# Optimization experiments

Hardware: AMD Instinct MI355X
Metric: run time of the kernel (lower is better)

## Reference

```python
import jax, jax.numpy as jnp
import numpy as np

XD = 64      # input_size
D = 512      # encoding_size
R = 512      # hidden_size (WFA rank)
MIX = 8      # mixture components
WIN = 4096   # window_size
INIT_STD = 0.1


def setup_inputs() -> dict:
    key = jax.random.key(0)
    ks = jax.random.split(key, 16)
    s = INIT_STD

    def lin(k, fan_out, fan_in):
        lim = 1.0 / np.sqrt(fan_in)
        kw, kb = jax.random.split(k)
        W = jax.random.uniform(kw, (fan_out, fan_in), jnp.float32, -lim, lim)
        b = jax.random.uniform(kb, (fan_out,), jnp.float32, -lim, lim)
        return W, b

    W1, b1 = lin(ks[3], D, XD)            # encoder_1: xd -> d
    W2, b2 = lin(ks[4], D, D)             # encoder_2: d -> d
    Wmu, bmu = lin(ks[5], MIX * XD, R)    # mu_out
    Wmu2, bmu2 = lin(ks[6], MIX * XD, MIX * XD)  # mu_out2
    Wsig, bsig = lin(ks[7], MIX * XD, R)  # sig_out
    Wal, bal = lin(ks[8], MIX, R)         # alpha_out

    return {
        "X": jax.random.normal(ks[0], (WIN, XD), jnp.float32),
        "prev": jax.nn.softmax(jax.random.uniform(ks[1], (1, R), jnp.float32), axis=1),
        "A": s * jax.random.normal(ks[2], (R, D, R), jnp.float32),
        "W1": W1, "b1": b1, "W2": W2, "b2": b2,
        "Wmu": Wmu, "bmu": bmu, "Wmu2": Wmu2, "bmu2": bmu2,
        "Wsig": Wsig, "bsig": bsig, "Wal": Wal, "bal": bal,
    }


def reference(X, prev, A, W1, b1, W2, b2, Wmu, bmu, Wmu2, bmu2, Wsig, bsig, Wal, bal):
    # prev is never updated inside the torch window loop, so all window_size-1
    # steps share the same prev -> vectorize over the window dimension T.
    cur = X[:-1]            # [T, xd]
    nxt = X[1:]             # [T, xd]

    # encoder: two linears with relu
    e = jax.nn.relu(cur @ W1.T + b1)        # [T, d]
    e = jax.nn.relu(e @ W2.T + b2)          # [T, d]

    # WFA transition: einsum('d,i,idj->j', enc_t, prev, A) for every t.
    # Contract prev with A once into a [d, r] transition matrix.
    B = jnp.einsum('i,idj->dj', prev.ravel(), A)   # [d, r]
    h = jax.nn.sigmoid(e @ B)                       # [T, r]

    # phi: mixture-density head evaluating log p(next | h)
    mu = ((h @ Wmu.T + bmu) @ Wmu2.T + bmu2).reshape(-1, MIX, XD)  # [T, K, xd]
    sig = jnp.exp(h @ Wsig.T + bsig).reshape(-1, MIX, XD)          # [T, K, xd]
    log_alpha = jax.nn.log_softmax(h @ Wal.T + bal, axis=-1)       # [T, K]

    z = (nxt[:, None, :] - mu) / sig
    log_comp = (-0.5 * jnp.sum(z * z, axis=-1)
                - jnp.sum(jnp.log(sig), axis=-1)
                - 0.5 * XD * jnp.log(2.0 * jnp.pi))                # [T, K]
    ll = jax.nn.logsumexp(log_alpha + log_comp, axis=-1)           # [T]

    # torch forward returns only the last step's result and the last hidden
    # state (detached) as the new prev.
    return ll[-1:], jax.lax.stop_gradient(h[-1:])
```

## Files before the change

### kernel.cpp

```cpp
#include <hip/hip_runtime.h>
#include <math.h>

#define NSLOT    8
#define WS_E     0
#define WS_E1    512
#define WS_HPRE  1024
#define WS_H     (WS_HPRE + NSLOT*512)
#define WS_T1    (WS_H + 512)
#define WS_SP    (WS_T1 + 512)
#define WS_MU    (WS_SP + 512)
#define WS_AL    (WS_MU + 512)

__global__ __launch_bounds__(256) void k_e1(const float* __restrict__ X,
    const float* __restrict__ W1, const float* __restrict__ b1,
    float* __restrict__ ws)
{
    int t = threadIdx.x, b = blockIdx.x;
    int w = t >> 6, l = t & 63;
    int r = b * 4 + w;
    float s = W1[(size_t)r * 64 + l] * X[4094 * 64 + l];
#pragma unroll
    for (int off = 32; off > 0; off >>= 1) s += __shfl_down(s, off);
    if (l == 0) ws[WS_E1 + r] = fmaxf(s + b1[r], 0.f);
    int gid = b * 256 + t;
    if (gid < NSLOT * 512) ws[WS_HPRE + gid] = 0.f;
}

__global__ __launch_bounds__(64) void k_e2(const float* __restrict__ W2,
    const float* __restrict__ b2, float* __restrict__ ws)
{
    int r = blockIdx.x, l = threadIdx.x;
    const float4* w4 = (const float4*)(W2 + (size_t)r * 512);
    const float4* x4 = (const float4*)(ws + WS_E1);
    float4 w0 = w4[2*l], w1 = w4[2*l+1];
    float4 x0 = x4[2*l], x1 = x4[2*l+1];
    float s = w0.x*x0.x + w0.y*x0.y + w0.z*x0.z + w0.w*x0.w
            + w1.x*x1.x + w1.y*x1.y + w1.z*x1.z + w1.w*x1.w;
#pragma unroll
    for (int off = 32; off > 0; off >>= 1) s += __shfl_down(s, off);
    if (l == 0) ws[WS_E + r] = fmaxf(s + b2[r], 0.f);
}

__global__ __launch_bounds__(256) void k_contract(const float* __restrict__ A,
    const float* __restrict__ prev, float* __restrict__ ws)
{
    __shared__ float cvals[136];
    __shared__ unsigned short idxs[136];
    __shared__ int cnts[2];
    __shared__ float4 comb[128];

    int t = threadIdx.x;
    int b = blockIdx.x;
    int i = b >> 2;
    int d0 = (b & 3) << 7;
    const float* e = ws + WS_E;

    float c = 0.f; bool nz = false;
    if (t < 128) {
        c = prev[i] * e[d0 + t];
        nz = (c != 0.f);
    }
    unsigned long long bm = __ballot(nz);
    int lane = t & 63;
    int w = t >> 6;
    if (t < 128 && lane == 0) cnts[w] = __popcll(bm);
    __syncthreads();
    if (nz) {
        int pos = __popcll(bm & ((1ull << lane) - 1)) + (w ? cnts[0] : 0);
        idxs[pos] = (unsigned short)t;
        cvals[pos] = c;
    }
    int nnz = cnts[0] + cnts[1];
    int nnzp = (nnz + 7) & ~7;
    if (t < 8 && nnz + t < nnzp) {
        cvals[nnz + t] = 0.f;
        idxs[nnz + t] = 0;
    }
    __syncthreads();

    int g  = t >> 7;
    int jj = t & 127;
    const float* Abase = A + ((size_t)i * 512 + d0) * 512 + (size_t)jj * 4;
    float4 acc = make_float4(0.f, 0.f, 0.f, 0.f);

#pragma unroll 2
    for (int k = g; k + 6 < nnzp; k += 8) {
        int dA = idxs[k], dB = idxs[k+2], dC = idxs[k+4], dD = idxs[k+6];
        float cA = cvals[k], cB = cvals[k+2], cC = cvals[k+4], cD = cvals[k+6];
        float4 a0 = *(const float4*)(Abase + ((size_t)dA << 9));
        float4 a1 = *(const float4*)(Abase + ((size_t)dB << 9));
        float4 a2 = *(const float4*)(Abase + ((size_t)dC << 9));
        float4 a3 = *(const float4*)(Abase + ((size_t)dD << 9));
        acc.x = fmaf(cA, a0.x, acc.x); acc.y = fmaf(cA, a0.y, acc.y);
        acc.z = fmaf(cA, a0.z, acc.z); acc.w = fmaf(cA, a0.w, acc.w);
        acc.x = fmaf(cB, a1.x, acc.x); acc.y = fmaf(cB, a1.y, acc.y);
        acc.z = fmaf(cB, a1.z, acc.z); acc.w = fmaf(cB, a1.w, acc.w);
        acc.x = fmaf(cC, a2.x, acc.x); acc.y = fmaf(cC, a2.y, acc.y);
        acc.z = fmaf(cC, a2.z, acc.z); acc.w = fmaf(cC, a2.w, acc.w);
        acc.x = fmaf(cD, a3.x, acc.x); acc.y = fmaf(cD, a3.y, acc.y);
        acc.z = fmaf(cD, a3.z, acc.z); acc.w = fmaf(cD, a3.w, acc.w);
    }

    if (g == 1) comb[jj] = acc;
    __syncthreads();
    if (g == 0) {
        float4 o = comb[jj];
        float* hp = ws + WS_HPRE + (size_t)(b & (NSLOT - 1)) * 512;
        int j = jj * 4;
        atomicAdd(&hp[j],     acc.x + o.x);
        atomicAdd(&hp[j + 1], acc.y + o.y);
        atomicAdd(&hp[j + 2], acc.z + o.z);
        atomicAdd(&hp[j + 3], acc.w + o.w);
    }
}

__global__ __launch_bounds__(512) void k_h(float* __restrict__ ws, float* __restrict__ out)
{
    int t = threadIdx.x;
    float s = 0.f;
#pragma unroll
    for (int s2 = 0; s2 < NSLOT; ++s2) s += ws[WS_HPRE + s2 * 512 + t];
    float h = 1.f / (1.f + expf(-s));
    ws[WS_H + t] = h;
    out[1 + t] = h;
}

__global__ __launch_bounds__(64) void k_mv3(const float* __restrict__ Wmu, const float* __restrict__ bmu,
    const float* __restrict__ Wsig, const float* __restrict__ bsig,
    const float* __restrict__ Wal, const float* __restrict__ bal,
    float* __restrict__ ws)
{
    int r = blockIdx.x;
    const float* Wrow; float bias; float* outp;
    if (r < 512)       { Wrow = Wmu  + (size_t)r * 512;          bias = bmu[r];          outp = ws + WS_T1 + r; }
    else if (r < 1024) { int rr = r - 512;  Wrow = Wsig + (size_t)rr * 512; bias = bsig[rr]; outp = ws + WS_SP + rr; }
    else               { int rr = r - 1024; Wrow = Wal  + (size_t)rr * 512; bias = bal[rr];  outp = ws + WS_AL + rr; }
    int l = threadIdx.x;
    const float4* W4 = (const float4*)Wrow;
    const float4* h4 = (const float4*)(ws + WS_H);
    float4 w0 = W4[2*l], w1 = W4[2*l+1];
    float4 h0 = h4[2*l], h1 = h4[2*l+1];
    float s = w0.x*h0.x + w0.y*h0.y + w0.z*h0.z + w0.w*h0.w
            + w1.x*h1.x + w1.y*h1.y + w1.z*h1.z + w1.w*h1.w;
#pragma unroll
    for (int off = 32; off > 0; off >>= 1) s += __shfl_down(s, off);
    if (l == 0) *outp = s + bias;
}

__global__ __launch_bounds__(64) void k_mv1(const float* __restrict__ W, const float* __restrict__ bvec,
    float* __restrict__ ws)
{
    int r = blockIdx.x;
    int l = threadIdx.x;
    const float4* W4 = (const float4*)(W + (size_t)r * 512);
    const float4* x4 = (const float4*)(ws + WS_T1);
    float4 w0 = W4[2*l], w1 = W4[2*l+1];
    float4 x0 = x4[2*l], x1 = x4[2*l+1];
    float s = w0.x*x0.x + w0.y*x0.y + w0.z*x0.z + w0.w*x0.w
            + w1.x*x1.x + w1.y*x1.y + w1.z*x1.z + w1.w*x1.w;
#pragma unroll
    for (int off = 32; off > 0; off >>= 1) s += __shfl_down(s, off);
    if (l == 0) ws[WS_MU + r] = s + bvec[r];
}

__global__ __launch_bounds__(512) void k_final(const float* __restrict__ X,
    float* __restrict__ ws, float* __restrict__ out)
{
    __shared__ float lc[8];
    int t = threadIdx.x;
    int m = t >> 6, x = t & 63;
    float nx = X[4095 * 64 + x];
    float mu = ws[WS_MU + t];
    float sp = ws[WS_SP + t];
    float z  = (nx - mu) * expf(-sp);
    float v  = 0.5f * z * z + sp;
#pragma unroll
    for (int off = 32; off > 0; off >>= 1) v += __shfl_down(v, off);
    if (x == 0) lc[m] = -v - 58.812066125099056f;
    __syncthreads();
    if (t == 0) {
        float al[8], g[8];
        float mx1 = -1e30f, mx2 = -1e30f;
#pragma unroll
        for (int q = 0; q < 8; ++q) {
            al[q] = ws[WS_AL + q];
            g[q]  = al[q] + lc[q];
            mx1 = fmaxf(mx1, al[q]);
            mx2 = fmaxf(mx2, g[q]);
        }
        float s1 = 0.f, s2 = 0.f;
#pragma unroll
        for (int q = 0; q < 8; ++q) { s1 += expf(al[q] - mx1); s2 += expf(g[q] - mx2); }
        out[0] = (mx2 + logf(s2)) - (mx1 + logf(s1));
    }
}

extern "C" void kernel_launch(void* const* d_in, const int* in_sizes, int n_in,
                              void* d_out, int out_size, void* d_ws, size_t ws_size,
                              hipStream_t stream)
{
    const float* X    = (const float*)d_in[0];
    const float* prev = (const float*)d_in[1];
    const float* A    = (const float*)d_in[2];
    const float* W1   = (const float*)d_in[3];
    const float* b1   = (const float*)d_in[4];
    const float* W2   = (const float*)d_in[5];
    const float* b2   = (const float*)d_in[6];
    const float* Wmu  = (const float*)d_in[7];
    const float* bmu  = (const float*)d_in[8];
    const float* Wmu2 = (const float*)d_in[9];
    const float* bmu2 = (const float*)d_in[10];
    const float* Wsig = (const float*)d_in[11];
    const float* bsig = (const float*)d_in[12];
    const float* Wal  = (const float*)d_in[13];
    const float* bal  = (const float*)d_in[14];
    float* out = (float*)d_out;
    float* ws  = (float*)d_ws;

    hipLaunchKernelGGL(k_e1,       dim3(128),  dim3(256), 0, stream, X, W1, b1, ws);
    hipLaunchKernelGGL(k_e2,       dim3(512),  dim3(64),  0, stream, W2, b2, ws);
    hipLaunchKernelGGL(k_contract, dim3(2048), dim3(256), 0, stream, A, prev, ws);
    hipLaunchKernelGGL(k_h,        dim3(1),    dim3(512), 0, stream, ws, out);
    hipLaunchKernelGGL(k_mv3,      dim3(1032), dim3(64),  0, stream, Wmu, bmu, Wsig, bsig, Wal, bal, ws);
    hipLaunchKernelGGL(k_mv1,      dim3(512),  dim3(64),  0, stream, Wmu2, bmu2, ws);
    hipLaunchKernelGGL(k_final,    dim3(1),    dim3(512), 0, stream, X, ws, out);
}
```

Before: 75.98 us.

## Fuse sigmoid into head matvec and final reduction into mu2 via atomics

```diff
diff --git a/kernel.cpp b/kernel.cpp
--- a/kernel.cpp
+++ b/kernel.cpp
@@ -1,15 +1,18 @@
 #include <hip/hip_runtime.h>
 #include <math.h>
+
+typedef float f32x4 __attribute__((ext_vector_type(4)));
 
 #define NSLOT    8
 #define WS_E     0
 #define WS_E1    512
 #define WS_HPRE  1024
-#define WS_H     (WS_HPRE + NSLOT*512)
-#define WS_T1    (WS_H + 512)
+#define WS_LC    (WS_HPRE + NSLOT*512)
+#define WS_CNT   (WS_LC + 8)
+#define WS_T1    (WS_CNT + 8)
 #define WS_SP    (WS_T1 + 512)
-#define WS_MU    (WS_SP + 512)
-#define WS_AL    (WS_MU + 512)
+#define WS_AL    (WS_SP + 512)
+#define WS_ZLEN  (NSLOT*512 + 16)
 
 __global__ __launch_bounds__(256) void k_e1(const float* __restrict__ X,
     const float* __restrict__ W1, const float* __restrict__ b1,
@@ -23,13 +26,15 @@
     for (int off = 32; off > 0; off >>= 1) s += __shfl_down(s, off);
     if (l == 0) ws[WS_E1 + r] = fmaxf(s + b1[r], 0.f);
     int gid = b * 256 + t;
-    if (gid < NSLOT * 512) ws[WS_HPRE + gid] = 0.f;
-}
-
-__global__ __launch_bounds__(64) void k_e2(const float* __restrict__ W2,
+    if (gid < WS_ZLEN) ws[WS_HPRE + gid] = 0.f;
+}
+
+__global__ __launch_bounds__(256) void k_e2(const float* __restrict__ W2,
     const float* __restrict__ b2, float* __restrict__ ws)
 {
-    int r = blockIdx.x, l = threadIdx.x;
+    int t = threadIdx.x, b = blockIdx.x;
+    int w = t >> 6, l = t & 63;
+    int r = b * 4 + w;
     const float4* w4 = (const float4*)(W2 + (size_t)r * 512);
     const float4* x4 = (const float4*)(ws + WS_E1);
     float4 w0 = w4[2*l], w1 = w4[2*l+1];
@@ -44,10 +49,10 @@
 __global__ __launch_bounds__(256) void k_contract(const float* __restrict__ A,
     const float* __restrict__ prev, float* __restrict__ ws)
 {
-    __shared__ float cvals[136];
-    __shared__ unsigned short idxs[136];
+    __shared__ float cvals[160];
+    __shared__ unsigned short idxs[160];
     __shared__ int cnts[2];
-    __shared__ float4 comb[128];
+    __shared__ float comb[512];
 
     int t = threadIdx.x;
     int b = blockIdx.x;
@@ -71,8 +76,8 @@
         cvals[pos] = c;
     }
     int nnz = cnts[0] + cnts[1];
-    int nnzp = (nnz + 7) & ~7;
-    if (t < 8 && nnz + t < nnzp) {
+    int nnzp = (nnz + 15) & ~15;
+    if (t < 16 && nnz + t < nnzp) {
         cvals[nnz + t] = 0.f;
         idxs[nnz + t] = 0;
     }
@@ -81,77 +86,81 @@
     int g  = t >> 7;
     int jj = t & 127;
     const float* Abase = A + ((size_t)i * 512 + d0) * 512 + (size_t)jj * 4;
-    float4 acc = make_float4(0.f, 0.f, 0.f, 0.f);
-
-#pragma unroll 2
-    for (int k = g; k + 6 < nnzp; k += 8) {
-        int dA = idxs[k], dB = idxs[k+2], dC = idxs[k+4], dD = idxs[k+6];
-        float cA = cvals[k], cB = cvals[k+2], cC = cvals[k+4], cD = cvals[k+6];
-        float4 a0 = *(const float4*)(Abase + ((size_t)dA << 9));
-        float4 a1 = *(const float4*)(Abase + ((size_t)dB << 9));
-        float4 a2 = *(const float4*)(Abase + ((size_t)dC << 9));
-        float4 a3 = *(const float4*)(Abase + ((size_t)dD << 9));
-        acc.x = fmaf(cA, a0.x, acc.x); acc.y = fmaf(cA, a0.y, acc.y);
-        acc.z = fmaf(cA, a0.z, acc.z); acc.w = fmaf(cA, a0.w, acc.w);
-        acc.x = fmaf(cB, a1.x, acc.x); acc.y = fmaf(cB, a1.y, acc.y);
-        acc.z = fmaf(cB, a1.z, acc.z); acc.w = fmaf(cB, a1.w, acc.w);
-        acc.x = fmaf(cC, a2.x, acc.x); acc.y = fmaf(cC, a2.y, acc.y);
-        acc.z = fmaf(cC, a2.z, acc.z); acc.w = fmaf(cC, a2.w, acc.w);
-        acc.x = fmaf(cD, a3.x, acc.x); acc.y = fmaf(cD, a3.y, acc.y);
-        acc.z = fmaf(cD, a3.z, acc.z); acc.w = fmaf(cD, a3.w, acc.w);
-    }
-
-    if (g == 1) comb[jj] = acc;
+    f32x4 acc = (f32x4)0.f;
+
+    for (int k = g; k + 14 < nnzp; k += 16) {
+        int i0 = idxs[k],    i1 = idxs[k+2],  i2 = idxs[k+4],  i3 = idxs[k+6];
+        int i4 = idxs[k+8],  i5 = idxs[k+10], i6 = idxs[k+12], i7 = idxs[k+14];
+        float c0 = cvals[k],    c1 = cvals[k+2],  c2 = cvals[k+4],  c3 = cvals[k+6];
+        float c4 = cvals[k+8],  c5 = cvals[k+10], c6 = cvals[k+12], c7 = cvals[k+14];
+        f32x4 a0 = __builtin_nontemporal_load((const f32x4*)(Abase + ((size_t)i0 << 9)));
+        f32x4 a1 = __builtin_nontemporal_load((const f32x4*)(Abase + ((size_t)i1 << 9)));
+        f32x4 a2 = __builtin_nontemporal_load((const f32x4*)(Abase + ((size_t)i2 << 9)));
+        f32x4 a3 = __builtin_nontemporal_load((const f32x4*)(Abase + ((size_t)i3 << 9)));
+        f32x4 a4 = __builtin_nontemporal_load((const f32x4*)(Abase + ((size_t)i4 << 9)));
+        f32x4 a5 = __builtin_nontemporal_load((const f32x4*)(Abase + ((size_t)i5 << 9)));
+        f32x4 a6 = __builtin_nontemporal_load((const f32x4*)(Abase + ((size_t)i6 << 9)));
+        f32x4 a7 = __builtin_nontemporal_load((const f32x4*)(Abase + ((size_t)i7 << 9)));
+        acc += c0 * a0; acc += c1 * a1; acc += c2 * a2; acc += c3 * a3;
+        acc += c4 * a4; acc += c5 * a5; acc += c6 * a6; acc += c7 * a7;
+    }
+
+    if (g == 1) { ((f32x4*)comb)[jj] = acc; }
     __syncthreads();
     if (g == 0) {
-        float4 o = comb[jj];
+        f32x4 o = ((f32x4*)comb)[jj];
+        acc += o;
         float* hp = ws + WS_HPRE + (size_t)(b & (NSLOT - 1)) * 512;
         int j = jj * 4;
-        atomicAdd(&hp[j],     acc.x + o.x);
-        atomicAdd(&hp[j + 1], acc.y + o.y);
-        atomicAdd(&hp[j + 2], acc.z + o.z);
-        atomicAdd(&hp[j + 3], acc.w + o.w);
-    }
-}
-
-__global__ __launch_bounds__(512) void k_h(float* __restrict__ ws, float* __restrict__ out)
-{
-    int t = threadIdx.x;
-    float s = 0.f;
-#pragma unroll
-    for (int s2 = 0; s2 < NSLOT; ++s2) s += ws[WS_HPRE + s2 * 512 + t];
-    float h = 1.f / (1.f + expf(-s));
-    ws[WS_H + t] = h;
-    out[1 + t] = h;
-}
-
-__global__ __launch_bounds__(64) void k_mv3(const float* __restrict__ Wmu, const float* __restrict__ bmu,
+        atomicAdd(&hp[j],     acc.x);
+        atomicAdd(&hp[j + 1], acc.y);
+        atomicAdd(&hp[j + 2], acc.z);
+        atomicAdd(&hp[j + 3], acc.w);
+    }
+}
+
+__global__ __launch_bounds__(64) void k_post1(const float* __restrict__ Wmu, const float* __restrict__ bmu,
     const float* __restrict__ Wsig, const float* __restrict__ bsig,
     const float* __restrict__ Wal, const float* __restrict__ bal,
-    float* __restrict__ ws)
-{
+    float* __restrict__ ws, float* __restrict__ out)
+{
+    __shared__ float h[512];
+    int t = threadIdx.x;
+#pragma unroll
+    for (int q = 0; q < 8; ++q) {
+        int j = q * 64 + t;
+        float s = 0.f;
+#pragma unroll
+        for (int s2 = 0; s2 < NSLOT; ++s2) s += ws[WS_HPRE + s2 * 512 + j];
+        h[j] = 1.f / (1.f + expf(-s));
+    }
+    __syncthreads();
+
     int r = blockIdx.x;
+    if (r == 1032) {
+#pragma unroll
+        for (int q = 0; q < 8; ++q) { int j = q * 64 + t; out[1 + j] = h[j]; }
+        return;
+    }
     const float* Wrow; float bias; float* outp;
-    if (r < 512)       { Wrow = Wmu  + (size_t)r * 512;          bias = bmu[r];          outp = ws + WS_T1 + r; }
+    if (r < 512)       { Wrow = Wmu  + (size_t)r * 512;           bias = bmu[r];           outp = ws + WS_T1 + r; }
     else if (r < 1024) { int rr = r - 512;  Wrow = Wsig + (size_t)rr * 512; bias = bsig[rr]; outp = ws + WS_SP + rr; }
     else               { int rr = r - 1024; Wrow = Wal  + (size_t)rr * 512; bias = bal[rr];  outp = ws + WS_AL + rr; }
-    int l = threadIdx.x;
     const float4* W4 = (const float4*)Wrow;
-    const float4* h4 = (const float4*)(ws + WS_H);
-    float4 w0 = W4[2*l], w1 = W4[2*l+1];
-    float4 h0 = h4[2*l], h1 = h4[2*l+1];
+    const float4* h4 = (const float4*)h;
+    float4 w0 = W4[2*t], w1 = W4[2*t+1];
+    float4 h0 = h4[2*t], h1 = h4[2*t+1];
     float s = w0.x*h0.x + w0.y*h0.y + w0.z*h0.z + w0.w*h0.w
             + w1.x*h1.x + w1.y*h1.y + w1.z*h1.z + w1.w*h1.w;
 #pragma unroll
     for (int off = 32; off > 0; off >>= 1) s += __shfl_down(s, off);
-    if (l == 0) *outp = s + bias;
-}
-
-__global__ __launch_bounds__(64) void k_mv1(const float* __restrict__ W, const float* __restrict__ bvec,
-    float* __restrict__ ws)
-{
-    int r = blockIdx.x;
-    int l = threadIdx.x;
+    if (t == 0) *outp = s + bias;
+}
+
+__global__ __launch_bounds__(64) void k_mu_final(const float* __restrict__ W, const float* __restrict__ bvec,
+    const float* __restrict__ X, float* __restrict__ ws, float* __restrict__ out)
+{
+    int r = blockIdx.x, l = threadIdx.x;
     const float4* W4 = (const float4*)(W + (size_t)r * 512);
     const float4* x4 = (const float4*)(ws + WS_T1);
     float4 w0 = W4[2*l], w1 = W4[2*l+1];
@@ -160,38 +169,31 @@
             + w1.x*x1.x + w1.y*x1.y + w1.z*x1.z + w1.w*x1.w;
 #pragma unroll
     for (int off = 32; off > 0; off >>= 1) s += __shfl_down(s, off);
-    if (l == 0) ws[WS_MU + r] = s + bvec[r];
-}
-
-__global__ __launch_bounds__(512) void k_final(const float* __restrict__ X,
-    float* __restrict__ ws, float* __restrict__ out)
-{
-    __shared__ float lc[8];
-    int t = threadIdx.x;
-    int m = t >> 6, x = t & 63;
-    float nx = X[4095 * 64 + x];
-    float mu = ws[WS_MU + t];
-    float sp = ws[WS_SP + t];
-    float z  = (nx - mu) * expf(-sp);
-    float v  = 0.5f * z * z + sp;
-#pragma unroll
-    for (int off = 32; off > 0; off >>= 1) v += __shfl_down(v, off);
-    if (x == 0) lc[m] = -v - 58.812066125099056f;
-    __syncthreads();
-    if (t == 0) {
-        float al[8], g[8];
-        float mx1 = -1e30f, mx2 = -1e30f;
-#pragma unroll
-        for (int q = 0; q < 8; ++q) {
-            al[q] = ws[WS_AL + q];
-            g[q]  = al[q] + lc[q];
-            mx1 = fmaxf(mx1, al[q]);
-            mx2 = fmaxf(mx2, g[q]);
+    if (l == 0) {
+        float mu = s + bvec[r];
+        int m = r >> 6, x = r & 63;
+        float nx = X[4095 * 64 + x];
+        float sp = ws[WS_SP + r];
+        float z  = (nx - mu) * expf(-sp);
+        atomicAdd(&ws[WS_LC + m], -(0.5f * z * z + sp));
+        __threadfence();
+        unsigned int done = atomicAdd((unsigned int*)(ws + WS_CNT), 1u);
+        if (done == 511) {
+            float al[8], g[8];
+            float mx1 = -1e30f, mx2 = -1e30f;
+#pragma unroll
+            for (int q = 0; q < 8; ++q) {
+                al[q] = ws[WS_AL + q];
+                float lc = atomicAdd(&ws[WS_LC + q], 0.f) - 58.812066125099056f;
+                g[q] = al[q] + lc;
+                mx1 = fmaxf(mx1, al[q]);
+                mx2 = fmaxf(mx2, g[q]);
+            }
+            float s1 = 0.f, s2 = 0.f;
+#pragma unroll
+            for (int q = 0; q < 8; ++q) { s1 += expf(al[q] - mx1); s2 += expf(g[q] - mx2); }
+            out[0] = (mx2 + logf(s2)) - (mx1 + logf(s1));
         }
-        float s1 = 0.f, s2 = 0.f;
-#pragma unroll
-        for (int q = 0; q < 8; ++q) { s1 += expf(al[q] - mx1); s2 += expf(g[q] - mx2); }
-        out[0] = (mx2 + logf(s2)) - (mx1 + logf(s1));
     }
 }
 
@@ -218,10 +220,8 @@
     float* ws  = (float*)d_ws;
 
     hipLaunchKernelGGL(k_e1,       dim3(128),  dim3(256), 0, stream, X, W1, b1, ws);
-    hipLaunchKernelGGL(k_e2,       dim3(512),  dim3(64),  0, stream, W2, b2, ws);
+    hipLaunchKernelGGL(k_e2,       dim3(128),  dim3(256), 0, stream, W2, b2, ws);
     hipLaunchKernelGGL(k_contract, dim3(2048), dim3(256), 0, stream, A, prev, ws);
-    hipLaunchKernelGGL(k_h,        dim3(1),    dim3(512), 0, stream, ws, out);
-    hipLaunchKernelGGL(k_mv3,      dim3(1032), dim3(64),  0, stream, Wmu, bmu, Wsig, bsig, Wal, bal, ws);
-    hipLaunchKernelGGL(k_mv1,      dim3(512),  dim3(64),  0, stream, Wmu2, bmu2, ws);
-    hipLaunchKernelGGL(k_final,    dim3(1),    dim3(512), 0, stream, X, ws, out);
-}
+    hipLaunchKernelGGL(k_post1,    dim3(1033), dim3(64),  0, stream, Wmu, bmu, Wsig, bsig, Wal, bal, ws, out);
+    hipLaunchKernelGGL(k_mu_final, dim3(512),  dim3(64),  0, stream, Wmu2, bmu2, X, ws, out);
+}
```

Result: slower. 85.10 us (+12.0%).
